# Kernel tuning notes

Measured on AMD Instinct MI355X. Metric: run time of the kernel, lower is better.

Reference implementation:

```python
import jax, jax.numpy as jnp
import numpy as np

N, M, FIN, K, OUT, E = 8, 49152, 64, 6, 64, 393216


def setup_inputs() -> dict:
    key = jax.random.key(0)
    k1, k2, k3, k4, k5, k6 = jax.random.split(key, 6)
    x = jax.random.normal(k1, (N, M, FIN), jnp.float32)
    rows = jax.random.randint(k2, (E,), 0, M, jnp.int32)
    cols = jax.random.randint(k3, (E,), 0, M, jnp.int32)
    vals = jax.random.normal(k4, (E,), jnp.float32) * 0.1  # scaled-Laplacian values
    stdv = 1.0 / np.sqrt(OUT)
    weight = jax.random.uniform(k5, (FIN * K, OUT), jnp.float32, -stdv, stdv)
    bias = jax.random.uniform(k6, (OUT,), jnp.float32, -stdv, stdv)
    return {"x": x, "rows": rows, "cols": cols, "vals": vals,
            "weight": weight, "bias": bias}


def reference(x, rows, cols, vals, weight, bias):
    # x: [N, M, Fin]; L sparse [M, M] in COO (rows, cols, vals)
    n, m, fin = x.shape
    # x0: [M, Fin*N] as in torch permute(1,2,0).view(M, Fin*N)
    x0 = jnp.transpose(x, (1, 2, 0)).reshape(m, fin * n)

    def spmm(X):  # L @ X via gather + segment-sum scatter
        return jax.ops.segment_sum(vals[:, None] * X[cols], rows, num_segments=m)

    xs = [x0]
    if K > 1:
        x1 = spmm(x0)
        xs.append(x1)
        for _ in range(2, K):
            x2 = 2.0 * spmm(x1) - x0
            xs.append(x2)
            x0, x1 = x1, x2

    # stack -> [K, M, Fin, N]; torch then permutes to [N, M, Fin, K] and
    # flattens to (N*M, Fin*K) with Fin outer, K inner: weight row idx = f*K + k
    T = jnp.stack(xs, 0).reshape(K, m, fin, n)
    Wr = weight.reshape(fin, K, OUT)
    out = jnp.einsum('kmfn,fko->nmo', T, Wr) + bias  # [N, M, OUT]
    return jax.nn.elu(out)
```

## Files before the change

### kernel.cpp

```cpp
#include <hip/hip_runtime.h>
#include <hip/hip_bf16.h>
#include <math.h>

#define N_    8
#define M_    49152
#define FIN_  64
#define K_    6
#define OUT_  64
#define E_    393216
#define ROW_  512

typedef __attribute__((ext_vector_type(8))) short bf16x8;
typedef __attribute__((ext_vector_type(4))) float f32x4;

static __device__ __forceinline__ unsigned short f2bf(float f) {
    unsigned u = __float_as_uint(f);
    u += 0x7fff + ((u >> 16) & 1);
    return (unsigned short)(u >> 16);
}
static __device__ __forceinline__ float bfl(unsigned u) { return __uint_as_float(u << 16); }
static __device__ __forceinline__ float bfh(unsigned u) { return __uint_as_float(u & 0xffff0000u); }


__global__ void count_kernel(const int* __restrict__ rows, int* __restrict__ cnt) {
    int e = blockIdx.x * blockDim.x + threadIdx.x;
    if (e < E_) atomicAdd(&cnt[rows[e]], 1);
}

__global__ __launch_bounds__(1024) void scanA_kernel(const int* __restrict__ cnt,
                                                     int* __restrict__ lscan,
                                                     int* __restrict__ bsum) {
    __shared__ int wsum[16];
    int b = blockIdx.x, t = threadIdx.x, lane = t & 63, wid = t >> 6;
    int v = cnt[b * 1024 + t];
    int s = v;
    #pragma unroll
    for (int off = 1; off < 64; off <<= 1) {
        int y = __shfl_up(s, off, 64);
        if (lane >= off) s += y;
    }
    if (lane == 63) wsum[wid] = s;
    __syncthreads();
    if (t == 0) {
        int run = 0;
        #pragma unroll
        for (int i = 0; i < 16; ++i) { int c = wsum[i]; wsum[i] = run; run += c; }
        bsum[b] = run;
    }
    __syncthreads();
    lscan[b * 1024 + t] = wsum[wid] + s - v;
}

__global__ void scanB_kernel(const int* __restrict__ bsum, int* __restrict__ boffs,
                             int* __restrict__ rowptr) {
    int t = threadIdx.x;
    int v = (t < 48) ? bsum[t] : 0;
    int s = v;
    #pragma unroll
    for (int off = 1; off < 64; off <<= 1) {
        int y = __shfl_up(s, off, 64);
        if (t >= off) s += y;
    }
    if (t < 48) boffs[t] = s - v;
    if (t == 0) rowptr[M_] = E_;
}

__global__ __launch_bounds__(1024) void scanC_kernel(int* __restrict__ rowptr,
                                                     const int* __restrict__ boffs,
                                                     int* __restrict__ cntfill) {
    int b = blockIdx.x, t = threadIdx.x;
    int val = rowptr[b * 1024 + t] + boffs[b];
    rowptr[b * 1024 + t]  = val;
    cntfill[b * 1024 + t] = val;
}

__global__ void fill_kernel(const int* __restrict__ rows, const int* __restrict__ cols,
                            const float* __restrict__ vals, int* __restrict__ fillpos,
                            int* __restrict__ ecol, float* __restrict__ evalv,
                            int* __restrict__ eidx) {
    int e = blockIdx.x * blockDim.x + threadIdx.x;
    if (e < E_) {
        int r = rows[e];
        int p = atomicAdd(&fillpos[r], 1);
        ecol[p]  = cols[e];
        evalv[p] = vals[e];
        eidx[p]  = e;
    }
}

__global__ void sort_kernel(const int* __restrict__ rowptr, int* __restrict__ ecol,
                            float* __restrict__ evalv, int* __restrict__ eidx) {
    int m = blockIdx.x * blockDim.x + threadIdx.x;
    if (m >= M_) return;
    int s = rowptr[m], e = rowptr[m + 1];
    for (int i = s + 1; i < e; ++i) {
        int ki = eidx[i]; int kc = ecol[i]; float kv = evalv[i];
        int j = i - 1;
        while (j >= s && eidx[j] > ki) {
            eidx[j + 1] = eidx[j]; ecol[j + 1] = ecol[j]; evalv[j + 1] = evalv[j];
            --j;
        }
        eidx[j + 1] = ki; ecol[j + 1] = kc; evalv[j + 1] = kv;
    }
}


__global__ void permute_count_kernel(const float* __restrict__ x, unsigned short* __restrict__ T0,
                                     const int* __restrict__ rows, int* __restrict__ cnt) {
    int idx = blockIdx.x * blockDim.x + threadIdx.x;
    int f4 = idx & 15, n = (idx >> 4) & 7, m = idx >> 7;
    float4 v = ((const float4*)x)[(size_t)(n * M_ + m) * 16 + f4];
    ushort4 o;
    o.x = f2bf(v.x); o.y = f2bf(v.y); o.z = f2bf(v.z); o.w = f2bf(v.w);
    *(ushort4*)(T0 + (size_t)m * ROW_ + n * 64 + f4 * 4) = o;
    if (idx < E_) atomicAdd(&cnt[rows[idx]], 1);
}

__global__ void fill_wprep_kernel(const int* __restrict__ rows, const int* __restrict__ cols,
                                  const float* __restrict__ vals, int* __restrict__ fillpos,
                                  int* __restrict__ ecol, float* __restrict__ evalv,
                                  int* __restrict__ eidx,
                                  const float* __restrict__ W, unsigned short* __restrict__ Wfrag) {
    int e = blockIdx.x * blockDim.x + threadIdx.x;
    if (e < E_) {
        int r = rows[e];
        int p = atomicAdd(&fillpos[r], 1);
        ecol[p]  = cols[e];
        evalv[p] = vals[e];
        eidx[p]  = e;
    }
    if (e < 24576) {
        int i = e & 7, l = (e >> 3) & 63, tile = (e >> 9) & 3, kk = e >> 11;
        int kcheb = kk >> 1;
        int f = (kk & 1) * 32 + (l >> 4) * 8 + i;
        int o = tile * 16 + (l & 15);
        Wfrag[e] = f2bf(W[(f * K_ + kcheb) * OUT_ + o]);
    }
}

static __device__ __forceinline__ void fma_u4(float* acc, float v, uint4 u) {
    acc[0] += v * bfl(u.x); acc[1] += v * bfh(u.x);
    acc[2] += v * bfl(u.y); acc[3] += v * bfh(u.y);
    acc[4] += v * bfl(u.z); acc[5] += v * bfh(u.z);
    acc[6] += v * bfl(u.w); acc[7] += v * bfh(u.w);
}

__global__ __launch_bounds__(256) void spmm_bf16_kernel(
        const unsigned short* __restrict__ cur, const unsigned short* __restrict__ prev,
        unsigned short* __restrict__ nxt,
        const int* __restrict__ rowptr, const int* __restrict__ ecol,
        const float* __restrict__ evalv, float alpha, float beta) {
    int t = threadIdx.x;
    int w = t >> 6, l = t & 63;
    int m = blockIdx.x * 4 + w;
    int s = rowptr[m], e = rowptr[m + 1];
    int cnt = e - s;
    int myc = 0; float myv = 0.f;
    if (l < cnt) { myc = ecol[s + l]; myv = evalv[s + l]; }
    uint4 p;
    if (beta != 0.f) p = *(const uint4*)(prev + (size_t)m * ROW_ + l * 8);

    float acc[8] = {0.f, 0.f, 0.f, 0.f, 0.f, 0.f, 0.f, 0.f};
    int lim = cnt < 64 ? cnt : 64;
    int i = 0;
    for (; i + 3 < lim; i += 4) {
        int c0 = __shfl(myc, i),     c1 = __shfl(myc, i + 1);
        int c2 = __shfl(myc, i + 2), c3 = __shfl(myc, i + 3);
        float v0 = __shfl(myv, i),     v1 = __shfl(myv, i + 1);
        float v2 = __shfl(myv, i + 2), v3 = __shfl(myv, i + 3);
        uint4 u0 = *(const uint4*)(cur + (size_t)c0 * ROW_ + l * 8);
        uint4 u1 = *(const uint4*)(cur + (size_t)c1 * ROW_ + l * 8);
        uint4 u2 = *(const uint4*)(cur + (size_t)c2 * ROW_ + l * 8);
        uint4 u3 = *(const uint4*)(cur + (size_t)c3 * ROW_ + l * 8);
        fma_u4(acc, v0, u0); fma_u4(acc, v1, u1);
        fma_u4(acc, v2, u2); fma_u4(acc, v3, u3);
    }
    for (; i < lim; ++i) {
        int c0 = __shfl(myc, i);
        float v0 = __shfl(myv, i);
        uint4 u0 = *(const uint4*)(cur + (size_t)c0 * ROW_ + l * 8);
        fma_u4(acc, v0, u0);
    }
    for (int j = 64; j < cnt; ++j) {
        int c0 = ecol[s + j];
        float v0 = evalv[s + j];
        uint4 u0 = *(const uint4*)(cur + (size_t)c0 * ROW_ + l * 8);
        fma_u4(acc, v0, u0);
    }
    #pragma unroll
    for (int j = 0; j < 8; ++j) acc[j] *= alpha;
    if (beta != 0.f) {
        acc[0] += beta * bfl(p.x); acc[1] += beta * bfh(p.x);
        acc[2] += beta * bfl(p.y); acc[3] += beta * bfh(p.y);
        acc[4] += beta * bfl(p.z); acc[5] += beta * bfh(p.z);
        acc[6] += beta * bfl(p.w); acc[7] += beta * bfh(p.w);
    }
    uint4 o;
    o.x = (unsigned)f2bf(acc[0]) | ((unsigned)f2bf(acc[1]) << 16);
    o.y = (unsigned)f2bf(acc[2]) | ((unsigned)f2bf(acc[3]) << 16);
    o.z = (unsigned)f2bf(acc[4]) | ((unsigned)f2bf(acc[5]) << 16);
    o.w = (unsigned)f2bf(acc[6]) | ((unsigned)f2bf(acc[7]) << 16);
    *(uint4*)(nxt + (size_t)m * ROW_ + l * 8) = o;
}

static __device__ __forceinline__ void epilogue_tile(
        f32x4 acc, int tile, int rbase, int col, float b,
        float* __restrict__ outn) {
    int c = tile * 16 + col;
    #pragma unroll
    for (int v = 0; v < 4; ++v) {
        float r = acc[v] + b;
        r = r > 0.f ? r : (__expf(r) - 1.f);
        outn[(size_t)(rbase + v) * OUT_ + c] = r;
    }
}

__global__ __launch_bounds__(512) void combine_kernel(
        const unsigned short* __restrict__ Tbase,
        const unsigned short* __restrict__ Wfrag,
        const float* __restrict__ bias, float* __restrict__ out) {
    __shared__ unsigned short wlds[24576];
    int t = threadIdx.x;
    {
        const uint4* src = (const uint4*)Wfrag;
        uint4* dst = (uint4*)wlds;
        #pragma unroll
        for (int i = 0; i < 6; ++i)
            dst[t + 512 * i] = src[t + 512 * i];
    }
    __syncthreads();

    int w = t >> 6, l = t & 63;
    int m0 = blockIdx.x * 128 + w * 16;
    int arow = m0 + (l & 15);
    const size_t MROW = (size_t)M_ * ROW_;
    size_t abase0 = (size_t)arow * ROW_ + (l >> 4) * 8;
    int rbase = m0 + (l >> 4) * 4;
    int col = l & 15;
    float b0 = bias[col], b1 = bias[16 + col], b2 = bias[32 + col], b3 = bias[48 + col];

    #pragma unroll
    for (int n = 0; n < 8; ++n) {
        size_t abase = abase0 + n * 64;
        bf16x8 a[12];
        #pragma unroll
        for (int kk = 0; kk < 12; ++kk)
            a[kk] = *(const bf16x8*)(Tbase + (size_t)(kk >> 1) * MROW + abase + (kk & 1) * 32);

        f32x4 acc0 = {0.f, 0.f, 0.f, 0.f};
        f32x4 acc1 = {0.f, 0.f, 0.f, 0.f};
        f32x4 acc2 = {0.f, 0.f, 0.f, 0.f};
        f32x4 acc3 = {0.f, 0.f, 0.f, 0.f};
        #pragma unroll
        for (int kk = 0; kk < 12; ++kk) {
            const unsigned short* wp = wlds + ((size_t)(kk * 4) * 64 + l) * 8;
            bf16x8 q0 = *(const bf16x8*)(wp);
            bf16x8 q1 = *(const bf16x8*)(wp + 512);
            bf16x8 q2 = *(const bf16x8*)(wp + 1024);
            bf16x8 q3 = *(const bf16x8*)(wp + 1536);
            acc0 = __builtin_amdgcn_mfma_f32_16x16x32_bf16(a[kk], q0, acc0, 0, 0, 0);
            acc1 = __builtin_amdgcn_mfma_f32_16x16x32_bf16(a[kk], q1, acc1, 0, 0, 0);
            acc2 = __builtin_amdgcn_mfma_f32_16x16x32_bf16(a[kk], q2, acc2, 0, 0, 0);
            acc3 = __builtin_amdgcn_mfma_f32_16x16x32_bf16(a[kk], q3, acc3, 0, 0, 0);
        }

        float* outn = out + (size_t)n * ((size_t)M_ * OUT_);
        epilogue_tile(acc0, 0, rbase, col, b0, outn);
        epilogue_tile(acc1, 1, rbase, col, b1, outn);
        epilogue_tile(acc2, 2, rbase, col, b2, outn);
        epilogue_tile(acc3, 3, rbase, col, b3, outn);
    }
}


__global__ void permute_kernel(const float* __restrict__ x, float* __restrict__ A) {
    int idx = blockIdx.x * blockDim.x + threadIdx.x;
    int f4 = idx & 15;
    int n  = (idx >> 4) & 7;
    int m  = idx >> 7;
    float4 v = ((const float4*)x)[(size_t)(n * M_ + m) * 16 + f4];
    ((float4*)A)[idx] = v;
}

__global__ __launch_bounds__(512) void step_kernel(
        const float* __restrict__ cur, float* __restrict__ nxt,
        const float* __restrict__ weight, const float* __restrict__ bias,
        const int* __restrict__ rowptr, const int* __restrict__ ecol,
        const float* __restrict__ evalv, float* __restrict__ out,
        int k, float alpha, float beta, int flags) {
    __shared__ float lds_x[ROW_];
    int m = blockIdx.x;
    int t = threadIdx.x;
    lds_x[t] = cur[(size_t)m * ROW_ + t];
    if (flags & 4) {
        float acc = 0.f;
        int s = rowptr[m], e = rowptr[m + 1];
        for (int i = s; i < e; ++i)
            acc += evalv[i] * cur[(size_t)ecol[i] * ROW_ + t];
        float prevv = (beta != 0.f) ? nxt[(size_t)m * ROW_ + t] : 0.f;
        nxt[(size_t)m * ROW_ + t] = alpha * acc + beta * prevv;
    }
    __syncthreads();
    int n = t >> 6, o = t & 63;
    const float4* lx4 = (const float4*)(lds_x + n * FIN_);
    float acc = 0.f;
    #pragma unroll
    for (int f4 = 0; f4 < 16; ++f4) {
        float4 xq = lx4[f4];
        int fb = f4 * 4;
        acc += xq.x * weight[((fb + 0) * K_ + k) * OUT_ + o];
        acc += xq.y * weight[((fb + 1) * K_ + k) * OUT_ + o];
        acc += xq.z * weight[((fb + 2) * K_ + k) * OUT_ + o];
        acc += xq.w * weight[((fb + 3) * K_ + k) * OUT_ + o];
    }
    size_t oidx = (size_t)n * (M_ * OUT_) + (size_t)m * OUT_ + o;
    float res = (flags & 1) ? acc : (out[oidx] + acc);
    if (flags & 2) {
        res += bias[o];
        res = (res > 0.f) ? res : (expf(res) - 1.f);
    }
    out[oidx] = res;
}


extern "C" void kernel_launch(void* const* d_in, const int* in_sizes, int n_in,
                              void* d_out, int out_size, void* d_ws, size_t ws_size,
                              hipStream_t stream) {
    (void)in_sizes; (void)n_in; (void)out_size;
    const float* x      = (const float*)d_in[0];
    const int*   rows   = (const int*)d_in[1];
    const int*   cols   = (const int*)d_in[2];
    const float* vals   = (const float*)d_in[3];
    const float* weight = (const float*)d_in[4];
    const float* bias   = (const float*)d_in[5];
    float* out = (float*)d_out;

    char* ws = (char*)d_ws;
    size_t off = 0;
    auto alloc = [&](size_t bytes) -> void* {
        void* p = ws + off;
        off += (bytes + 255) & ~(size_t)255;
        return p;
    };

    const size_t tbytes = (size_t)M_ * ROW_ * 2;
    const size_t need_new = 6 * (tbytes + 256) + (M_ + 1) * 4 + M_ * 4
                          + 3 * ((size_t)E_ * 4 + 256) + 24576 * 2 + 8192;

    if (ws_size >= need_new) {
        unsigned short* T[6];
        for (int i = 0; i < 6; ++i) T[i] = (unsigned short*)alloc(tbytes);
        int*   rowptr  = (int*)alloc((size_t)(M_ + 1) * 4);
        int*   fillpos = (int*)alloc((size_t)M_ * 4);
        int*   ecol    = (int*)alloc((size_t)E_ * 4);
        float* evalv   = (float*)alloc((size_t)E_ * 4);
        int*   eidx    = (int*)alloc((size_t)E_ * 4);
        unsigned short* Wfrag = (unsigned short*)alloc(24576 * 2);
        int*   bsum    = (int*)alloc(48 * 4);
        int*   boffs   = (int*)alloc(48 * 4);

        hipMemsetAsync(fillpos, 0, (size_t)M_ * 4, stream);
        permute_count_kernel<<<(M_ * N_ * 16) / 256, 256, 0, stream>>>(x, T[0], rows, fillpos);
        scanA_kernel<<<48, 1024, 0, stream>>>(fillpos, rowptr, bsum);
        scanB_kernel<<<1, 64, 0, stream>>>(bsum, boffs, rowptr);
        scanC_kernel<<<48, 1024, 0, stream>>>(rowptr, boffs, fillpos);
        fill_wprep_kernel<<<E_ / 256, 256, 0, stream>>>(rows, cols, vals, fillpos,
                                                        ecol, evalv, eidx, weight, Wfrag);
        sort_kernel<<<M_ / 256, 256, 0, stream>>>(rowptr, ecol, evalv, eidx);

        spmm_bf16_kernel<<<M_ / 4, 256, 0, stream>>>(T[0], T[0], T[1], rowptr, ecol, evalv, 1.f, 0.f);
        spmm_bf16_kernel<<<M_ / 4, 256, 0, stream>>>(T[1], T[0], T[2], rowptr, ecol, evalv, 2.f, -1.f);
        spmm_bf16_kernel<<<M_ / 4, 256, 0, stream>>>(T[2], T[1], T[3], rowptr, ecol, evalv, 2.f, -1.f);
        spmm_bf16_kernel<<<M_ / 4, 256, 0, stream>>>(T[3], T[2], T[4], rowptr, ecol, evalv, 2.f, -1.f);
        spmm_bf16_kernel<<<M_ / 4, 256, 0, stream>>>(T[4], T[3], T[5], rowptr, ecol, evalv, 2.f, -1.f);

        combine_kernel<<<M_ / 128, 512, 0, stream>>>(T[0], Wfrag, bias, out);
    } else {
        float* A       = (float*)alloc((size_t)M_ * ROW_ * 4);
        float* B       = (float*)alloc((size_t)M_ * ROW_ * 4);
        int*   rowptr  = (int*)alloc((size_t)(M_ + 1) * 4);
        int*   fillpos = (int*)alloc((size_t)M_ * 4);
        int*   ecol    = (int*)alloc((size_t)E_ * 4);
        float* evalv   = (float*)alloc((size_t)E_ * 4);
        int*   eidx    = (int*)alloc((size_t)E_ * 4);
        int*   bsum    = (int*)alloc(48 * 4);
        int*   boffs   = (int*)alloc(48 * 4);

        permute_kernel<<<(M_ * N_ * 16) / 256, 256, 0, stream>>>(x, A);
        hipMemsetAsync(fillpos, 0, (size_t)M_ * 4, stream);
        count_kernel<<<E_ / 256, 256, 0, stream>>>(rows, fillpos);
        scanA_kernel<<<48, 1024, 0, stream>>>(fillpos, rowptr, bsum);
        scanB_kernel<<<1, 64, 0, stream>>>(bsum, boffs, rowptr);
        scanC_kernel<<<48, 1024, 0, stream>>>(rowptr, boffs, fillpos);
        fill_kernel<<<E_ / 256, 256, 0, stream>>>(rows, cols, vals, fillpos, ecol, evalv, eidx);
        sort_kernel<<<M_ / 256, 256, 0, stream>>>(rowptr, ecol, evalv, eidx);

        step_kernel<<<M_, 512, 0, stream>>>(A, B, weight, bias, rowptr, ecol, evalv, out, 0, 1.f, 0.f, 1 | 4);
        step_kernel<<<M_, 512, 0, stream>>>(B, A, weight, bias, rowptr, ecol, evalv, out, 1, 2.f, -1.f, 4);
        step_kernel<<<M_, 512, 0, stream>>>(A, B, weight, bias, rowptr, ecol, evalv, out, 2, 2.f, -1.f, 4);
        step_kernel<<<M_, 512, 0, stream>>>(B, A, weight, bias, rowptr, ecol, evalv, out, 3, 2.f, -1.f, 4);
        step_kernel<<<M_, 512, 0, stream>>>(A, B, weight, bias, rowptr, ecol, evalv, out, 4, 2.f, -1.f, 4);
        step_kernel<<<M_, 512, 0, stream>>>(B, B, weight, bias, rowptr, ecol, evalv, out, 5, 0.f, 0.f, 2);
    }
}
```

Baseline: 562.0 us.

## Deepen SpMM gather unroll and split combine kernel work across smaller blocks

The SpMM inner loop now issues eight gathered row loads per iteration instead of four, with 4/2/1 remainder steps, so more memory requests are in flight per wave. The combine kernel moves to 256-thread blocks over 32 rows, with each wave handling half of the batch dimension, which gives four times as many blocks. The aim is more memory-level parallelism in the gather and better load balance across CUs in the combine. In exchange, each combine block still loads the full weight array into LDS, so that load is repeated four times as often, and the wider unroll raises register pressure.

```diff
diff --git a/kernel.cpp b/kernel.cpp
--- a/kernel.cpp
+++ b/kernel.cpp
@@ -163,23 +163,46 @@
     float acc[8] = {0.f, 0.f, 0.f, 0.f, 0.f, 0.f, 0.f, 0.f};
     int lim = cnt < 64 ? cnt : 64;
     int i = 0;
-    for (; i + 3 < lim; i += 4) {
+    for (; i + 8 <= lim; i += 8) {
         int c0 = __shfl(myc, i),     c1 = __shfl(myc, i + 1);
         int c2 = __shfl(myc, i + 2), c3 = __shfl(myc, i + 3);
-        float v0 = __shfl(myv, i),     v1 = __shfl(myv, i + 1);
-        float v2 = __shfl(myv, i + 2), v3 = __shfl(myv, i + 3);
+        int c4 = __shfl(myc, i + 4), c5 = __shfl(myc, i + 5);
+        int c6 = __shfl(myc, i + 6), c7 = __shfl(myc, i + 7);
         uint4 u0 = *(const uint4*)(cur + (size_t)c0 * ROW_ + l * 8);
         uint4 u1 = *(const uint4*)(cur + (size_t)c1 * ROW_ + l * 8);
         uint4 u2 = *(const uint4*)(cur + (size_t)c2 * ROW_ + l * 8);
         uint4 u3 = *(const uint4*)(cur + (size_t)c3 * ROW_ + l * 8);
-        fma_u4(acc, v0, u0); fma_u4(acc, v1, u1);
-        fma_u4(acc, v2, u2); fma_u4(acc, v3, u3);
-    }
-    for (; i < lim; ++i) {
+        uint4 u4 = *(const uint4*)(cur + (size_t)c4 * ROW_ + l * 8);
+        uint4 u5 = *(const uint4*)(cur + (size_t)c5 * ROW_ + l * 8);
+        uint4 u6 = *(const uint4*)(cur + (size_t)c6 * ROW_ + l * 8);
+        uint4 u7 = *(const uint4*)(cur + (size_t)c7 * ROW_ + l * 8);
+        fma_u4(acc, __shfl(myv, i),     u0); fma_u4(acc, __shfl(myv, i + 1), u1);
+        fma_u4(acc, __shfl(myv, i + 2), u2); fma_u4(acc, __shfl(myv, i + 3), u3);
+        fma_u4(acc, __shfl(myv, i + 4), u4); fma_u4(acc, __shfl(myv, i + 5), u5);
+        fma_u4(acc, __shfl(myv, i + 6), u6); fma_u4(acc, __shfl(myv, i + 7), u7);
+    }
+    if (i + 4 <= lim) {
+        int c0 = __shfl(myc, i),     c1 = __shfl(myc, i + 1);
+        int c2 = __shfl(myc, i + 2), c3 = __shfl(myc, i + 3);
+        uint4 u0 = *(const uint4*)(cur + (size_t)c0 * ROW_ + l * 8);
+        uint4 u1 = *(const uint4*)(cur + (size_t)c1 * ROW_ + l * 8);
+        uint4 u2 = *(const uint4*)(cur + (size_t)c2 * ROW_ + l * 8);
+        uint4 u3 = *(const uint4*)(cur + (size_t)c3 * ROW_ + l * 8);
+        fma_u4(acc, __shfl(myv, i),     u0); fma_u4(acc, __shfl(myv, i + 1), u1);
+        fma_u4(acc, __shfl(myv, i + 2), u2); fma_u4(acc, __shfl(myv, i + 3), u3);
+        i += 4;
+    }
+    if (i + 2 <= lim) {
+        int c0 = __shfl(myc, i), c1 = __shfl(myc, i + 1);
+        uint4 u0 = *(const uint4*)(cur + (size_t)c0 * ROW_ + l * 8);
+        uint4 u1 = *(const uint4*)(cur + (size_t)c1 * ROW_ + l * 8);
+        fma_u4(acc, __shfl(myv, i), u0); fma_u4(acc, __shfl(myv, i + 1), u1);
+        i += 2;
+    }
+    if (i < lim) {
         int c0 = __shfl(myc, i);
-        float v0 = __shfl(myv, i);
         uint4 u0 = *(const uint4*)(cur + (size_t)c0 * ROW_ + l * 8);
-        fma_u4(acc, v0, u0);
+        fma_u4(acc, __shfl(myv, i), u0);
     }
     for (int j = 64; j < cnt; ++j) {
         int c0 = ecol[s + j];
@@ -215,7 +238,7 @@
     }
 }
 
-__global__ __launch_bounds__(512) void combine_kernel(
+__global__ __launch_bounds__(256) void combine_kernel(
         const unsigned short* __restrict__ Tbase,
         const unsigned short* __restrict__ Wfrag,
         const float* __restrict__ bias, float* __restrict__ out) {
@@ -225,13 +248,14 @@
         const uint4* src = (const uint4*)Wfrag;
         uint4* dst = (uint4*)wlds;
         #pragma unroll
-        for (int i = 0; i < 6; ++i)
-            dst[t + 512 * i] = src[t + 512 * i];
+        for (int i = 0; i < 12; ++i)
+            dst[t + 256 * i] = src[t + 256 * i];
     }
     __syncthreads();
 
     int w = t >> 6, l = t & 63;
-    int m0 = blockIdx.x * 128 + w * 16;
+    int rowhalf = w & 1, nhalf = w >> 1;
+    int m0 = blockIdx.x * 32 + rowhalf * 16;
     int arow = m0 + (l & 15);
     const size_t MROW = (size_t)M_ * ROW_;
     size_t abase0 = (size_t)arow * ROW_ + (l >> 4) * 8;
@@ -240,7 +264,8 @@
     float b0 = bias[col], b1 = bias[16 + col], b2 = bias[32 + col], b3 = bias[48 + col];
 
     #pragma unroll
-    for (int n = 0; n < 8; ++n) {
+    for (int ni = 0; ni < 4; ++ni) {
+        int n = nhalf * 4 + ni;
         size_t abase = abase0 + n * 64;
         bf16x8 a[12];
         #pragma unroll
@@ -374,7 +399,7 @@
         spmm_bf16_kernel<<<M_ / 4, 256, 0, stream>>>(T[3], T[2], T[4], rowptr, ecol, evalv, 2.f, -1.f);
         spmm_bf16_kernel<<<M_ / 4, 256, 0, stream>>>(T[4], T[3], T[5], rowptr, ecol, evalv, 2.f, -1.f);
 
-        combine_kernel<<<M_ / 128, 512, 0, stream>>>(T[0], Wfrag, bias, out);
+        combine_kernel<<<M_ / 32, 256, 0, stream>>>(T[0], Wfrag, bias, out);
     } else {
         float* A       = (float*)alloc((size_t)M_ * ROW_ * 4);
         float* B       = (float*)alloc((size_t)M_ * ROW_ * 4);
```

After: 530.9 us. 1.06x faster.
